# Kernel optimization log

Measured on AMD Instinct MI355X. Metric: run time of the kernel, lower is better.

## Reference

```python
import jax, jax.numpy as jnp
import numpy as np

N_POINTS = 1048576
LEVELS = 16
LOG2T = 19
TABLE_SIZE = 1 << LOG2T  # 524288
FEAT = 2
MIN_RES = 16.0
MAX_RES = 512.0


def setup_inputs() -> dict:
    key = jax.random.key(0)
    kx, kt = jax.random.split(key)
    bounding_box = jnp.array([[-1.5, -1.5, -1.5], [1.5, 1.5, 1.5]], dtype=jnp.float32)
    # sample mostly inside the box, a few points slightly outside to exercise clamp/keep_mask
    x = jax.random.uniform(kx, (N_POINTS, 3), dtype=jnp.float32, minval=-1.6, maxval=1.6)
    # torch init: uniform(-1e-4, 1e-4) per level embedding table
    tables = jax.random.uniform(kt, (LEVELS, TABLE_SIZE, FEAT), dtype=jnp.float32,
                                minval=-1e-4, maxval=1e-4)
    return {"x": x, "bounding_box": bounding_box, "tables": tables}


def _hash_encode(x, bounding_box, tables):
    min_b, max_b = bounding_box[0], bounding_box[1]  # [3]
    # keep_mask: point unchanged by clamping in every dim
    keep_mask = jnp.all((x >= min_b) & (x <= max_b), axis=-1)
    xc = jnp.clip(x, min_b, max_b)
    u = (xc - min_b) / (max_b - min_b)  # normalized to [0,1], [N,3]

    b = jnp.exp((jnp.log(MAX_RES) - jnp.log(MIN_RES)) / (LEVELS - 1))
    PI = jnp.array([1, 2654435761, 805459861], dtype=jnp.uint32)
    HASH_MASK = jnp.uint32(TABLE_SIZE - 1)
    # 8 corner offsets in (i,j,k) order matching the torch module
    offs = jnp.array([[i, j, k] for i in (0, 1) for j in (0, 1) for k in (0, 1)],
                     dtype=jnp.int32)  # [8,3]

    outs = []
    for level in range(LEVELS):
        Nl = jnp.floor(MIN_RES * b ** level)            # scalar resolution
        box_size = (max_b - min_b) / Nl                 # [3]
        grid = jnp.floor(u * Nl).astype(jnp.int32)      # [N,3] min-corner grid coords
        vmin = grid.astype(x.dtype) * box_size + min_b  # [N,3]
        vmax = vmin + box_size                          # [N,3]
        corners = (grid[:, None, :] + offs[None, :, :]).astype(jnp.uint32)  # [N,8,3]
        # spatial hash: xor of coord*prime, wrap-around in uint32 matches low bits of torch int64
        h = (corners[..., 0] * PI[0]) ^ (corners[..., 1] * PI[1]) ^ (corners[..., 2] * PI[2])
        idx = (h & HASH_MASK).astype(jnp.int32)         # [N,8]
        emb = tables[level][idx]                        # gather -> [N,8,F]
        # trilinear interpolation; note: uses ORIGINAL (unclamped) x, as in the torch code
        w = (x - vmin) / (vmax - vmin)                  # [N,3]
        wx, wy, wz = w[:, 0:1], w[:, 1:2], w[:, 2:3]
        c00 = emb[:, 0] * (1 - wx) + emb[:, 4] * wx
        c01 = emb[:, 1] * (1 - wx) + emb[:, 5] * wx
        c10 = emb[:, 2] * (1 - wx) + emb[:, 6] * wx
        c11 = emb[:, 3] * (1 - wx) + emb[:, 7] * wx
        c0 = c00 * (1 - wy) + c10 * wy
        c1 = c01 * (1 - wy) + c11 * wy
        outs.append(c0 * (1 - wz) + c1 * wz)            # [N,F]
    return jnp.concatenate(outs, axis=-1), keep_mask    # [N, L*F], [N]


def reference(x, bounding_box, tables):
    return _hash_encode(x, bounding_box, tables)
```

## Files before the change

### kernel.cpp

```cpp
#include <hip/hip_runtime.h>

#define NPTS   1048576
#define NLEV   16
#define TSIZE  (1u << 19)
#define HMASK  (TSIZE - 1u)
#define NBUCK  32768

__device__ __constant__ float NLF_TAB[16] = {
    16.f, 20.f, 25.f, 32.f, 40.f, 50.f, 64.f, 80.f,
    101.f, 128.f, 161.f, 203.f, 256.f, 322.f, 406.f, 512.f};

__device__ __forceinline__ unsigned spread5(unsigned x) {
    x &= 0x1F;
    x = (x | (x << 8)) & 0x100F;
    x = (x | (x << 4)) & 0x10C3;
    x = (x | (x << 2)) & 0x1249;
    return x;
}

__device__ __forceinline__ unsigned morton_key(float u0, float u1, float u2) {
    unsigned k0 = min(31u, (unsigned)(u0 * 32.0f));
    unsigned k1 = min(31u, (unsigned)(u1 * 32.0f));
    unsigned k2 = min(31u, (unsigned)(u2 * 32.0f));
    return (spread5(k0) << 2) | (spread5(k1) << 1) | spread5(k2);
}

__device__ __forceinline__ void uvw(float x0, float x1, float x2,
                                    float* u0, float* u1, float* u2) {
    const float mn = -1.5f, mx = 1.5f, rng = 3.0f;
    *u0 = (fminf(fmaxf(x0, mn), mx) - mn) / rng;
    *u1 = (fminf(fmaxf(x1, mn), mx) - mn) / rng;
    *u2 = (fminf(fmaxf(x2, mn), mx) - mn) / rng;
}

__device__ __forceinline__ void level_lerp(
    float x0, float x1, float x2, float u0, float u1, float u2,
    float Nl, const float2* __restrict__ tab, float* r0, float* r1)
{
#pragma clang fp contract(off)
    const float mn = -1.5f, rng = 3.0f;
    const float box = rng / Nl;

    int g0 = (int)floorf(u0 * Nl);
    int g1 = (int)floorf(u1 * Nl);
    int g2 = (int)floorf(u2 * Nl);

    float vmin0 = (float)g0 * box + mn;
    float vmin1 = (float)g1 * box + mn;
    float vmin2 = (float)g2 * box + mn;

    float den0 = (vmin0 + box) - vmin0;
    float den1 = (vmin1 + box) - vmin1;
    float den2 = (vmin2 + box) - vmin2;

    float wx = (x0 - vmin0) / den0;
    float wy = (x1 - vmin1) / den1;
    float wz = (x2 - vmin2) / den2;

    unsigned hx0 = (unsigned)g0;
    unsigned hx1 = (unsigned)(g0 + 1);
    unsigned hy0 = (unsigned)g1       * 2654435761u;
    unsigned hy1 = (unsigned)(g1 + 1) * 2654435761u;
    unsigned hz0 = (unsigned)g2       * 805459861u;
    unsigned hz1 = (unsigned)(g2 + 1) * 805459861u;

    float2 e000 = tab[(hx0 ^ hy0 ^ hz0) & HMASK];
    float2 e001 = tab[(hx0 ^ hy0 ^ hz1) & HMASK];
    float2 e010 = tab[(hx0 ^ hy1 ^ hz0) & HMASK];
    float2 e011 = tab[(hx0 ^ hy1 ^ hz1) & HMASK];
    float2 e100 = tab[(hx1 ^ hy0 ^ hz0) & HMASK];
    float2 e101 = tab[(hx1 ^ hy0 ^ hz1) & HMASK];
    float2 e110 = tab[(hx1 ^ hy1 ^ hz0) & HMASK];
    float2 e111 = tab[(hx1 ^ hy1 ^ hz1) & HMASK];

    float omx = 1.0f - wx, omy = 1.0f - wy, omz = 1.0f - wz;
    {
        float c00 = e000.x * omx + e100.x * wx;
        float c01 = e001.x * omx + e101.x * wx;
        float c10 = e010.x * omx + e110.x * wx;
        float c11 = e011.x * omx + e111.x * wx;
        float c0  = c00 * omy + c10 * wy;
        float c1  = c01 * omy + c11 * wy;
        *r0 = c0 * omz + c1 * wz;
    }
    {
        float c00 = e000.y * omx + e100.y * wx;
        float c01 = e001.y * omx + e101.y * wx;
        float c10 = e010.y * omx + e110.y * wx;
        float c11 = e011.y * omx + e111.y * wx;
        float c0  = c00 * omy + c10 * wy;
        float c1  = c01 * omy + c11 * wy;
        *r1 = c0 * omz + c1 * wz;
    }
}


__global__ __launch_bounds__(256)
void hist_kernel(const float* __restrict__ xin, unsigned* __restrict__ hist)
{
    int p = blockIdx.x * 256 + threadIdx.x;
    if (p >= NPTS) return;
    float x0 = xin[3 * p], x1 = xin[3 * p + 1], x2 = xin[3 * p + 2];
    float u0, u1, u2; uvw(x0, x1, x2, &u0, &u1, &u2);
    atomicAdd(&hist[morton_key(u0, u1, u2)], 1u);
}

__global__ __launch_bounds__(1024)
void scan_kernel(unsigned* __restrict__ hist, unsigned* __restrict__ cursor)
{
    __shared__ unsigned part[1024];
    int t = threadIdx.x;
    unsigned local[32];
    unsigned s = 0;
#pragma unroll
    for (int i = 0; i < 32; ++i) { local[i] = hist[t * 32 + i]; s += local[i]; }
    part[t] = s;
    __syncthreads();
    for (int off = 1; off < 1024; off <<= 1) {
        unsigned v = (t >= off) ? part[t - off] : 0;
        __syncthreads();
        part[t] += v;
        __syncthreads();
    }
    unsigned base = (t == 0) ? 0u : part[t - 1];
#pragma unroll
    for (int i = 0; i < 32; ++i) {
        cursor[t * 32 + i] = base;
        base += local[i];
    }
}

__global__ __launch_bounds__(256)
void scatter_kernel(const float* __restrict__ xin,
                    unsigned* __restrict__ cursor,
                    unsigned* __restrict__ sidx,
                    float4* __restrict__ sx4)
{
    int p = blockIdx.x * 256 + threadIdx.x;
    if (p >= NPTS) return;
    float x0 = xin[3 * p], x1 = xin[3 * p + 1], x2 = xin[3 * p + 2];
    float u0, u1, u2; uvw(x0, x1, x2, &u0, &u1, &u2);
    unsigned pos = atomicAdd(&cursor[morton_key(u0, u1, u2)], 1u);
    sidx[pos] = (unsigned)p;
    sx4[pos] = make_float4(x0, x1, x2, 0.0f);
}


__global__ __launch_bounds__(256)
void coarse_sorted(const unsigned* __restrict__ sidx,
                   const float4* __restrict__ sx4,
                   const float* __restrict__ tables,
                   float* __restrict__ out)
{
#pragma clang fp contract(off)
    int s = blockIdx.x * 256 + threadIdx.x;
    if (s >= NPTS) return;
    unsigned p = sidx[s];
    float4 xv = sx4[s];
    float u0, u1, u2; uvw(xv.x, xv.y, xv.z, &u0, &u1, &u2);

    float res[16];
#pragma unroll
    for (int l = 0; l < 8; ++l) {
        const float2* tab = (const float2*)tables + (size_t)l * TSIZE;
        level_lerp(xv.x, xv.y, xv.z, u0, u1, u2, NLF_TAB[l], tab,
                   &res[2 * l], &res[2 * l + 1]);
    }

    float4* orow = (float4*)(out + (size_t)p * 32);
#pragma unroll
    for (int i = 0; i < 4; ++i)
        orow[i] = make_float4(res[4 * i + 0], res[4 * i + 1],
                              res[4 * i + 2], res[4 * i + 3]);
}

__global__ __launch_bounds__(256)
void mid_sorted(const unsigned* __restrict__ sidx,
                const float4* __restrict__ sx4,
                const float* __restrict__ tables,
                float* __restrict__ out)
{
#pragma clang fp contract(off)
    int s = blockIdx.x * 256 + threadIdx.x;
    if (s >= NPTS) return;
    unsigned p = sidx[s];
    float4 xv = sx4[s];
    float u0, u1, u2; uvw(xv.x, xv.y, xv.z, &u0, &u1, &u2);

    float r[4];
    {
        const float2* tab = (const float2*)tables + (size_t)8 * TSIZE;
        level_lerp(xv.x, xv.y, xv.z, u0, u1, u2, NLF_TAB[8], tab, &r[0], &r[1]);
    }
    {
        const float2* tab = (const float2*)tables + (size_t)9 * TSIZE;
        level_lerp(xv.x, xv.y, xv.z, u0, u1, u2, NLF_TAB[9], tab, &r[2], &r[3]);
    }
    *(float4*)(out + (size_t)p * 32 + 16) = make_float4(r[0], r[1], r[2], r[3]);
}

template<int L, bool WRITE_MASK>
__global__ __launch_bounds__(256)
void fine_kernel(const float* __restrict__ xin,
                 const float* __restrict__ tables,
                 float* __restrict__ out)
{
#pragma clang fp contract(off)
    int p = blockIdx.x * 256 + threadIdx.x;
    if (p >= NPTS) return;
    float x0 = xin[3 * p], x1 = xin[3 * p + 1], x2 = xin[3 * p + 2];
    float u0, u1, u2; uvw(x0, x1, x2, &u0, &u1, &u2);

    const float2* tab = (const float2*)tables + (size_t)L * TSIZE;
    float r0, r1;
    level_lerp(x0, x1, x2, u0, u1, u2, NLF_TAB[L], tab, &r0, &r1);
    *(float2*)(out + (size_t)p * 32 + 2 * L) = make_float2(r0, r1);

    if (WRITE_MASK) {
        const float mn = -1.5f, mx = 1.5f;
        float keep = (x0 >= mn && x0 <= mx &&
                      x1 >= mn && x1 <= mx &&
                      x2 >= mn && x2 <= mx) ? 1.0f : 0.0f;
        out[(size_t)NPTS * 32 + p] = keep;
    }
}


__global__ __launch_bounds__(256)
void coarse_kernel(const float* __restrict__ xin,
                   const float* __restrict__ tables,
                   float* __restrict__ out)
{
#pragma clang fp contract(off)
    int p = blockIdx.x * 256 + threadIdx.x;
    if (p >= NPTS) return;
    float x0 = xin[3 * p], x1 = xin[3 * p + 1], x2 = xin[3 * p + 2];
    float u0, u1, u2; uvw(x0, x1, x2, &u0, &u1, &u2);

    float res[16];
#pragma unroll
    for (int l = 0; l < 8; ++l) {
        const float2* tab = (const float2*)tables + (size_t)l * TSIZE;
        level_lerp(x0, x1, x2, u0, u1, u2, NLF_TAB[l], tab,
                   &res[2 * l], &res[2 * l + 1]);
    }
    float4* orow = (float4*)(out + (size_t)p * 32);
#pragma unroll
    for (int i = 0; i < 4; ++i)
        orow[i] = make_float4(res[4 * i + 0], res[4 * i + 1],
                              res[4 * i + 2], res[4 * i + 3]);
}

extern "C" void kernel_launch(void* const* d_in, const int* in_sizes, int n_in,
                              void* d_out, int out_size, void* d_ws, size_t ws_size,
                              hipStream_t stream) {
    const float* x      = (const float*)d_in[0];
    const float* tables = (const float*)d_in[2];
    float* out = (float*)d_out;

    int n = in_sizes[0] / 3;
    int blocks = (n + 255) / 256;

    const size_t HIST_B   = (size_t)NBUCK * 4;
    const size_t SIDX_OFF = 131072;
    const size_t SX4_OFF  = SIDX_OFF + (size_t)NPTS * 4;
    const size_t NEEDED   = SX4_OFF + (size_t)NPTS * 16;

    if (ws_size >= NEEDED) {
        unsigned* hist = (unsigned*)d_ws;
        unsigned* sidx = (unsigned*)((char*)d_ws + SIDX_OFF);
        float4*   sx4  = (float4*)((char*)d_ws + SX4_OFF);

        hipMemsetAsync(hist, 0, HIST_B, stream);
        hist_kernel<<<blocks, 256, 0, stream>>>(x, hist);
        scan_kernel<<<1, 1024, 0, stream>>>(hist, hist);
        scatter_kernel<<<blocks, 256, 0, stream>>>(x, hist, sidx, sx4);

        coarse_sorted<<<blocks, 256, 0, stream>>>(sidx, sx4, tables, out);
        mid_sorted<<<blocks, 256, 0, stream>>>(sidx, sx4, tables, out);
    } else {
        coarse_kernel<<<blocks, 256, 0, stream>>>(x, tables, out);
        fine_kernel< 8, false><<<blocks, 256, 0, stream>>>(x, tables, out);
        fine_kernel< 9, false><<<blocks, 256, 0, stream>>>(x, tables, out);
    }

    fine_kernel<10, true ><<<blocks, 256, 0, stream>>>(x, tables, out);
    fine_kernel<11, false><<<blocks, 256, 0, stream>>>(x, tables, out);
    fine_kernel<12, false><<<blocks, 256, 0, stream>>>(x, tables, out);
    fine_kernel<13, false><<<blocks, 256, 0, stream>>>(x, tables, out);
    fine_kernel<14, false><<<blocks, 256, 0, stream>>>(x, tables, out);
    fine_kernel<15, false><<<blocks, 256, 0, stream>>>(x, tables, out);
}
```

Baseline: 479.8 us.

## Fuse Morton sort stages into fine-level kernels to remove standalone passes

The histogram pass is folded into the level-15 fine kernel, the prefix scan runs as an extra block appended to the level-14 kernel, and the scatter runs as extra blocks of the level-13 kernel. This removes two separate full passes over the points and the serial single-block scan launch, overlapping the sort preparation with gather work. The scan block now uses 256 threads with 128 buckets each, and relies on block scheduling order: the scan block only runs correctly if the fine-15 kernel has completed, which stream ordering guarantees. The scatter blocks within fine13 likewise depend on the scan having finished in the previous launch.

```diff
diff --git a/kernel.cpp b/kernel.cpp
--- a/kernel.cpp
+++ b/kernel.cpp
@@ -95,49 +95,89 @@
 }
 
 
-__global__ __launch_bounds__(256)
-void hist_kernel(const float* __restrict__ xin, unsigned* __restrict__ hist)
+template<int L, bool DO_HIST, bool DO_MASK>
+__device__ __forceinline__ void fine_body(
+    const float* __restrict__ xin, const float* __restrict__ tables,
+    float* __restrict__ out, unsigned* __restrict__ hist, int p)
+{
+#pragma clang fp contract(off)
+    float x0 = xin[3 * p], x1 = xin[3 * p + 1], x2 = xin[3 * p + 2];
+    float u0, u1, u2; uvw(x0, x1, x2, &u0, &u1, &u2);
+
+    if (DO_HIST)
+        atomicAdd(&hist[morton_key(u0, u1, u2)], 1u);
+
+    const float2* tab = (const float2*)tables + (size_t)L * TSIZE;
+    float r0, r1;
+    level_lerp(x0, x1, x2, u0, u1, u2, NLF_TAB[L], tab, &r0, &r1);
+    *(float2*)(out + (size_t)p * 32 + 2 * L) = make_float2(r0, r1);
+
+    if (DO_MASK) {
+        const float mn = -1.5f, mx = 1.5f;
+        float keep = (x0 >= mn && x0 <= mx &&
+                      x1 >= mn && x1 <= mx &&
+                      x2 >= mn && x2 <= mx) ? 1.0f : 0.0f;
+        out[(size_t)NPTS * 32 + p] = keep;
+    }
+}
+
+template<int L, bool DO_HIST, bool DO_MASK>
+__global__ __launch_bounds__(256)
+void fine_kernel(const float* __restrict__ xin,
+                 const float* __restrict__ tables,
+                 float* __restrict__ out,
+                 unsigned* __restrict__ hist)
 {
     int p = blockIdx.x * 256 + threadIdx.x;
     if (p >= NPTS) return;
-    float x0 = xin[3 * p], x1 = xin[3 * p + 1], x2 = xin[3 * p + 2];
-    float u0, u1, u2; uvw(x0, x1, x2, &u0, &u1, &u2);
-    atomicAdd(&hist[morton_key(u0, u1, u2)], 1u);
-}
-
-__global__ __launch_bounds__(1024)
-void scan_kernel(unsigned* __restrict__ hist, unsigned* __restrict__ cursor)
-{
-    __shared__ unsigned part[1024];
+    fine_body<L, DO_HIST, DO_MASK>(xin, tables, out, hist, p);
+}
+
+__global__ __launch_bounds__(256)
+void fine14_scan(const float* __restrict__ xin,
+                 const float* __restrict__ tables,
+                 float* __restrict__ out,
+                 unsigned* __restrict__ hist)
+{
+    __shared__ unsigned part[256];
+    if (blockIdx.x < 4096) {
+        int p = blockIdx.x * 256 + threadIdx.x;
+        fine_body<14, false, false>(xin, tables, out, hist, p);
+        return;
+    }
     int t = threadIdx.x;
-    unsigned local[32];
     unsigned s = 0;
-#pragma unroll
-    for (int i = 0; i < 32; ++i) { local[i] = hist[t * 32 + i]; s += local[i]; }
+    for (int i = 0; i < 128; ++i) s += hist[t * 128 + i];
     part[t] = s;
     __syncthreads();
-    for (int off = 1; off < 1024; off <<= 1) {
+    for (int off = 1; off < 256; off <<= 1) {
         unsigned v = (t >= off) ? part[t - off] : 0;
         __syncthreads();
         part[t] += v;
         __syncthreads();
     }
     unsigned base = (t == 0) ? 0u : part[t - 1];
-#pragma unroll
-    for (int i = 0; i < 32; ++i) {
-        cursor[t * 32 + i] = base;
-        base += local[i];
-    }
-}
-
-__global__ __launch_bounds__(256)
-void scatter_kernel(const float* __restrict__ xin,
+    for (int i = 0; i < 128; ++i) {
+        unsigned c = hist[t * 128 + i];
+        hist[t * 128 + i] = base;
+        base += c;
+    }
+}
+
+__global__ __launch_bounds__(256)
+void fine13_scatter(const float* __restrict__ xin,
+                    const float* __restrict__ tables,
+                    float* __restrict__ out,
                     unsigned* __restrict__ cursor,
                     unsigned* __restrict__ sidx,
                     float4* __restrict__ sx4)
 {
-    int p = blockIdx.x * 256 + threadIdx.x;
-    if (p >= NPTS) return;
+    if (blockIdx.x < 4096) {
+        int p = blockIdx.x * 256 + threadIdx.x;
+        fine_body<13, false, false>(xin, tables, out, (unsigned*)nullptr, p);
+        return;
+    }
+    int p = (blockIdx.x - 4096) * 256 + threadIdx.x;
     float x0 = xin[3 * p], x1 = xin[3 * p + 1], x2 = xin[3 * p + 2];
     float u0, u1, u2; uvw(x0, x1, x2, &u0, &u1, &u2);
     unsigned pos = atomicAdd(&cursor[morton_key(u0, u1, u2)], 1u);
@@ -199,32 +239,6 @@
     *(float4*)(out + (size_t)p * 32 + 16) = make_float4(r[0], r[1], r[2], r[3]);
 }
 
-template<int L, bool WRITE_MASK>
-__global__ __launch_bounds__(256)
-void fine_kernel(const float* __restrict__ xin,
-                 const float* __restrict__ tables,
-                 float* __restrict__ out)
-{
-#pragma clang fp contract(off)
-    int p = blockIdx.x * 256 + threadIdx.x;
-    if (p >= NPTS) return;
-    float x0 = xin[3 * p], x1 = xin[3 * p + 1], x2 = xin[3 * p + 2];
-    float u0, u1, u2; uvw(x0, x1, x2, &u0, &u1, &u2);
-
-    const float2* tab = (const float2*)tables + (size_t)L * TSIZE;
-    float r0, r1;
-    level_lerp(x0, x1, x2, u0, u1, u2, NLF_TAB[L], tab, &r0, &r1);
-    *(float2*)(out + (size_t)p * 32 + 2 * L) = make_float2(r0, r1);
-
-    if (WRITE_MASK) {
-        const float mn = -1.5f, mx = 1.5f;
-        float keep = (x0 >= mn && x0 <= mx &&
-                      x1 >= mn && x1 <= mx &&
-                      x2 >= mn && x2 <= mx) ? 1.0f : 0.0f;
-        out[(size_t)NPTS * 32 + p] = keep;
-    }
-}
-
 
 __global__ __launch_bounds__(256)
 void coarse_kernel(const float* __restrict__ xin,
@@ -272,22 +286,25 @@
         float4*   sx4  = (float4*)((char*)d_ws + SX4_OFF);
 
         hipMemsetAsync(hist, 0, HIST_B, stream);
-        hist_kernel<<<blocks, 256, 0, stream>>>(x, hist);
-        scan_kernel<<<1, 1024, 0, stream>>>(hist, hist);
-        scatter_kernel<<<blocks, 256, 0, stream>>>(x, hist, sidx, sx4);
+
+        fine_kernel<15, true , false><<<blocks, 256, 0, stream>>>(x, tables, out, hist);
+        fine14_scan<<<blocks + 1, 256, 0, stream>>>(x, tables, out, hist);
+        fine13_scatter<<<2 * blocks, 256, 0, stream>>>(x, tables, out, hist, sidx, sx4);
+        fine_kernel<12, false, false><<<blocks, 256, 0, stream>>>(x, tables, out, hist);
+        fine_kernel<11, false, false><<<blocks, 256, 0, stream>>>(x, tables, out, hist);
+        fine_kernel<10, false, true ><<<blocks, 256, 0, stream>>>(x, tables, out, hist);
 
         coarse_sorted<<<blocks, 256, 0, stream>>>(sidx, sx4, tables, out);
         mid_sorted<<<blocks, 256, 0, stream>>>(sidx, sx4, tables, out);
     } else {
         coarse_kernel<<<blocks, 256, 0, stream>>>(x, tables, out);
-        fine_kernel< 8, false><<<blocks, 256, 0, stream>>>(x, tables, out);
-        fine_kernel< 9, false><<<blocks, 256, 0, stream>>>(x, tables, out);
-    }
-
-    fine_kernel<10, true ><<<blocks, 256, 0, stream>>>(x, tables, out);
-    fine_kernel<11, false><<<blocks, 256, 0, stream>>>(x, tables, out);
-    fine_kernel<12, false><<<blocks, 256, 0, stream>>>(x, tables, out);
-    fine_kernel<13, false><<<blocks, 256, 0, stream>>>(x, tables, out);
-    fine_kernel<14, false><<<blocks, 256, 0, stream>>>(x, tables, out);
-    fine_kernel<15, false><<<blocks, 256, 0, stream>>>(x, tables, out);
-}
+        fine_kernel< 8, false, false><<<blocks, 256, 0, stream>>>(x, tables, out, nullptr);
+        fine_kernel< 9, false, false><<<blocks, 256, 0, stream>>>(x, tables, out, nullptr);
+        fine_kernel<10, false, true ><<<blocks, 256, 0, stream>>>(x, tables, out, nullptr);
+        fine_kernel<11, false, false><<<blocks, 256, 0, stream>>>(x, tables, out, nullptr);
+        fine_kernel<12, false, false><<<blocks, 256, 0, stream>>>(x, tables, out, nullptr);
+        fine_kernel<13, false, false><<<blocks, 256, 0, stream>>>(x, tables, out, nullptr);
+        fine_kernel<14, false, false><<<blocks, 256, 0, stream>>>(x, tables, out, nullptr);
+        fine_kernel<15, false, false><<<blocks, 256, 0, stream>>>(x, tables, out, nullptr);
+    }
+}
```

New measurement: 455.8 us. 5.0% less time.
